# Kernel optimization log

Hardware: AMD Instinct MI355X
Metric: run time of the kernel (lower is better)

## Reference

```python
import jax, jax.numpy as jnp
import numpy as np
import math

B, N, F0, HID, OUT, K = 8, 2048, 128, 64, 16, 10


def setup_inputs() -> dict:
    key = jax.random.key(0)
    ks = jax.random.split(key, 6)
    X = jax.random.normal(ks[0], (B, N, F0), dtype=jnp.float32)
    # Row-stochastic dense 'rescaled Laplacian': spectrum inside unit disk,
    # so K-th order Bernstein polynomial stays numerically stable.
    A = jax.random.uniform(ks[1], (N, N), dtype=jnp.float32)
    L = A / jnp.sum(A, axis=1, keepdims=True)
    W1 = jax.random.normal(ks[2], (F0, HID), dtype=jnp.float32) / np.float32(np.sqrt(F0))
    b1 = jnp.zeros((HID,), dtype=jnp.float32)
    W2 = jax.random.normal(ks[3], (HID, OUT), dtype=jnp.float32) / np.float32(np.sqrt(HID))
    b2 = jnp.zeros((OUT,), dtype=jnp.float32)
    theta = 0.02 * jax.random.normal(ks[4], (K + 1,), dtype=jnp.float32)
    return {"X": X, "L": L, "W1": W1, "b1": b1, "W2": W2, "b2": b2,
            "theta": theta, "dp": 0}


def _bern_filter(Hf, L, theta, binom):
    # g(L) Hf = sum_i theta_i C(K,i) L^i (I-L)^{K-i} Hf
    # Computed by applying L / (I-L) directly to the (B,N,F) features
    # (mathematically identical to forming the NxN basis matrices).
    Lap = lambda Y: jnp.einsum('vw,bwf->bvf', L, Y)
    ys = [Hf]                       # ys[k] = (I-L)^k Hf
    for _ in range(K):
        ys.append(ys[-1] - Lap(ys[-1]))
    a = theta * binom               # (K+1,)
    # Horner in L: r = a_K Hf; r <- L r + a_i (I-L)^{K-i} Hf
    r = a[K] * Hf
    for i in range(K - 1, -1, -1):
        r = Lap(r) + a[i] * ys[K - i]
    return r


def reference(X, L, W1, b1, W2, b2, theta, dp):
    binom = jnp.asarray([math.comb(K, i) for i in range(K + 1)], dtype=X.dtype)
    # dropout with p=dp=0 is identity
    Hf = jax.nn.relu(X @ W1 + b1)          # (B, N, HID)
    Hf = _bern_filter(Hf, L, theta, binom) # (B, N, HID)
    Hg = jnp.mean(Hf, axis=1)              # (B, HID)
    logits = Hg @ W2 + b2                  # (B, OUT)
    return logits
```

## Files before the change

kernel.cpp:

```cpp
#include <hip/hip_runtime.h>

#define NN     2048
#define F0D    128
#define HIDD   64
#define OUTD   16
#define KDEG   10
#define NCHAIN 128
#define COLS   16

typedef unsigned long long u64;
typedef unsigned int u32;

#define CTAG(j) (0xC0DE0000u + (u32)(j))
#define HTAG    0xBEEF0001u

static __device__ __forceinline__ u64 ld_ag(const u64* p) {
    return __hip_atomic_load(p, __ATOMIC_RELAXED, __HIP_MEMORY_SCOPE_AGENT);
}
static __device__ __forceinline__ void st_ag(u64* p, u64 v) {
    __hip_atomic_store(p, v, __ATOMIC_RELAXED, __HIP_MEMORY_SCOPE_AGENT);
}
static __device__ __forceinline__ u64 pk(u32 tag, float x) {
    return ((u64)tag << 32) | (u64)__float_as_uint(x);
}


__global__ __launch_bounds__(256, 1) void k_fused(
    const float* __restrict__ X, const float* __restrict__ L,
    const float* __restrict__ W1, const float* __restrict__ b1,
    const float* __restrict__ W2, const float* __restrict__ b2,
    const float* __restrict__ theta, float* __restrict__ out,
    float* __restrict__ ws)
{
    u64* bpW0  = (u64*)ws;
    u64* bpW1  = bpW0 + NN;
    u64* weffW = bpW0 + 2 * NN;
    u64* HpW   = bpW0 + 3 * NN;

    __shared__ union {
        struct { float Lt[NN * COLS]; float xs[NN]; float redf[4][16]; float cbv[16]; } mv;
        struct { float W1t[64][132]; float redm[16][65]; float wv[64]; } hd;
    } sm;

    const int g = blockIdx.x;
    const int t = threadIdx.x;

    if (g < NCHAIN) {
        const int u0 = g * COLS;

        if (t <= KDEG) {
            const float C10[11] = {1,10,45,120,210,252,210,120,45,10,1};
            float acc = 0.f;
            for (int i = 0; i <= t; ++i) {
                int n = KDEG - i, r = t - i;
                long long cm = 1;
                for (int s = 1; s <= r; ++s) cm = cm * (n - r + s) / s;
                float term = theta[i] * C10[i] * (float)cm;
                if ((t - i) & 1) term = -term;
                acc += term;
            }
            sm.mv.cbv[t] = acc;
        }

        const float4* L4  = (const float4*)L;
        float4*       Lt4 = (float4*)sm.mv.Lt;
        #pragma unroll 16
        for (int i = 0; i < 32; ++i) {
            int idx = t + 256 * i;
            int v = idx >> 2, qc = idx & 3;
            Lt4[idx] = L4[(size_t)v * (NN / 4) + (u0 >> 2) + qc];
        }
        __syncthreads();

        float wacc = 0.f;
        for (int j = 1; j <= KDEG; ++j) {
            float pprev = 1.0f;
            if (j > 1) {
                const u64* src = ((j - 1) & 1) ? bpW1 : bpW0;
                const u32 tag = CTAG(j - 1);
                const int base = t * 8;
                u64 vb[8];
                u32 need = 0xFFu;
                while (need) {
                    #pragma unroll
                    for (int i = 0; i < 8; ++i) {
                        if (need & (1u << i)) {
                            u64 x = ld_ag(&src[base + i]);
                            if ((u32)(x >> 32) == tag) { vb[i] = x; need &= ~(1u << i); }
                        }
                    }
                    if (need) __builtin_amdgcn_s_sleep(1);
                }
                #pragma unroll
                for (int i = 0; i < 8; ++i)
                    sm.mv.xs[base + i] = __uint_as_float((u32)vb[i]);
                __syncthreads();
                if (t < COLS) pprev = sm.mv.xs[u0 + t];
            }

            const int qc = t & 3, r = t >> 2;
            float4 acc = make_float4(0.f, 0.f, 0.f, 0.f);
            #pragma unroll 8
            for (int k = 0; k < 32; ++k) {
                int v = r + 64 * k;
                float xv = (j == 1) ? 1.0f : sm.mv.xs[v];
                float4 lv = Lt4[v * 4 + qc];
                acc.x += lv.x * xv; acc.y += lv.y * xv;
                acc.z += lv.z * xv; acc.w += lv.w * xv;
            }
            #pragma unroll
            for (int m = 4; m <= 32; m <<= 1) {
                acc.x += __shfl_xor(acc.x, m); acc.y += __shfl_xor(acc.y, m);
                acc.z += __shfl_xor(acc.z, m); acc.w += __shfl_xor(acc.w, m);
            }
            int lane = t & 63, wid = t >> 6;
            if (lane < 4) *(float4*)&sm.mv.redf[wid][lane * 4] = acc;
            __syncthreads();

            if (t < COLS) {
                float s = sm.mv.redf[0][t] + sm.mv.redf[1][t]
                        + sm.mv.redf[2][t] + sm.mv.redf[3][t];
                wacc += sm.mv.cbv[j - 1] * pprev;
                if (j < KDEG) {
                    u64* dst = (j & 1) ? bpW1 : bpW0;
                    st_ag(&dst[u0 + t], pk(CTAG(j), s));
                } else {
                    st_ag(&weffW[u0 + t],
                          pk(CTAG(KDEG), wacc + sm.mv.cbv[KDEG] * s));
                }
            }
        }

        if (g == 0) {
            const float inv = 1.0f / (float)NN;
            float s2[2];
            const int idx0 = t * 2;
            #pragma unroll
            for (int e = 0; e < 2; ++e) {
                int idx = idx0 + e;
                int b = idx >> 6, h = idx & 63;
                const u64* base = &HpW[(size_t)(b * 32) * 64 + h];
                u32 rem = 0xFFFFFFFFu;
                float ssum = 0.f;
                while (rem) {
                    for (int vc = 0; vc < 32; ++vc) {
                        if (rem & (1u << vc)) {
                            u64 x = ld_ag(base + (size_t)vc * 64);
                            if ((u32)(x >> 32) == HTAG) {
                                ssum += __uint_as_float((u32)x);
                                rem &= ~(1u << vc);
                            }
                        }
                    }
                    if (rem) __builtin_amdgcn_s_sleep(4);
                }
                s2[e] = ssum * inv;
            }
            sm.mv.xs[idx0] = s2[0];
            sm.mv.xs[idx0 + 1] = s2[1];
            __syncthreads();
            if (t < 128) {
                int o = t & 15, bb = t >> 4;
                float a3 = b2[o];
                #pragma unroll
                for (int h = 0; h < HIDD; ++h)
                    a3 += sm.mv.xs[bb * 64 + h] * W2[h * 16 + o];
                out[bb * 16 + o] = a3;
            }
        }
        return;
    }

    const int u = g - NCHAIN;
    const int vchunk = u & 31, bA = u >> 5, bB = bA + 4;

    for (int i = t; i < F0D * HIDD; i += 256) {
        int f = i >> 6, h = i & 63;
        sm.hd.W1t[h][f] = W1[i];
    }
    __syncthreads();

    const int hg = t & 15, vg = t >> 4;
    const int vbase = vchunk * 64 + vg * 4;
    const float* XA = X + ((size_t)bA * NN + vbase) * F0D;
    const float* XB = X + ((size_t)bB * NN + vbase) * F0D;
    float accA[4][4] = {}, accB[4][4] = {};
    for (int f = 0; f < F0D; f += 4) {
        float4 xa[4], xb[4];
        #pragma unroll
        for (int i = 0; i < 4; ++i) {
            xa[i] = *(const float4*)(XA + (size_t)i * F0D + f);
            xb[i] = *(const float4*)(XB + (size_t)i * F0D + f);
        }
        #pragma unroll
        for (int jj = 0; jj < 4; ++jj) {
            float4 wr = *(const float4*)(&sm.hd.W1t[hg + 16 * jj][f]);
            #pragma unroll
            for (int i = 0; i < 4; ++i) {
                accA[i][jj] += xa[i].x * wr.x + xa[i].y * wr.y
                             + xa[i].z * wr.z + xa[i].w * wr.w;
                accB[i][jj] += xb[i].x * wr.x + xb[i].y * wr.y
                             + xb[i].z * wr.z + xb[i].w * wr.w;
            }
        }
    }

    if (t < 64) {
        const u64* wp = &weffW[vchunk * 64 + t];
        u64 x = ld_ag(wp);
        while ((u32)(x >> 32) != CTAG(KDEG)) {
            __builtin_amdgcn_s_sleep(16);
            x = ld_ag(wp);
        }
        sm.hd.wv[t] = __uint_as_float((u32)x);
    }
    __syncthreads();

    float hsA[4] = {0.f,0.f,0.f,0.f}, hsB[4] = {0.f,0.f,0.f,0.f};
    #pragma unroll
    for (int i = 0; i < 4; ++i) {
        float we = sm.hd.wv[vg * 4 + i];
        #pragma unroll
        for (int jj = 0; jj < 4; ++jj) {
            float rA = accA[i][jj] + b1[hg + 16 * jj];
            float rB = accB[i][jj] + b1[hg + 16 * jj];
            rA = rA > 0.f ? rA : 0.f;
            rB = rB > 0.f ? rB : 0.f;
            hsA[jj] += rA * we;
            hsB[jj] += rB * we;
        }
    }
    #pragma unroll
    for (int jj = 0; jj < 4; ++jj) sm.hd.redm[vg][hg + 16 * jj] = hsA[jj];
    __syncthreads();
    if (t < 64) {
        float s = 0.f;
        #pragma unroll
        for (int i = 0; i < 16; ++i) s += sm.hd.redm[i][t];
        st_ag(&HpW[(size_t)(bA * 32 + vchunk) * 64 + t], pk(HTAG, s));
    }
    __syncthreads();
    #pragma unroll
    for (int jj = 0; jj < 4; ++jj) sm.hd.redm[vg][hg + 16 * jj] = hsB[jj];
    __syncthreads();
    if (t < 64) {
        float s = 0.f;
        #pragma unroll
        for (int i = 0; i < 16; ++i) s += sm.hd.redm[i][t];
        st_ag(&HpW[(size_t)(bB * 32 + vchunk) * 64 + t], pk(HTAG, s));
    }
}

extern "C" void kernel_launch(void* const* d_in, const int* in_sizes, int n_in,
                              void* d_out, int out_size, void* d_ws, size_t ws_size,
                              hipStream_t stream) {
    const float* X     = (const float*)d_in[0];
    const float* L     = (const float*)d_in[1];
    const float* W1    = (const float*)d_in[2];
    const float* b1    = (const float*)d_in[3];
    const float* W2    = (const float*)d_in[4];
    const float* b2    = (const float*)d_in[5];
    const float* theta = (const float*)d_in[6];
    float* outp = (float*)d_out;
    float* wsp  = (float*)d_ws;

    hipLaunchKernelGGL(k_fused, dim3(256), dim3(256), 0, stream,
                       X, L, W1, b1, W2, b2, theta, outp, wsp);
}
```

Baseline: 140.4 us.

## Replace tagged 64-bit value polling with per-block flags and plain data buffers

Cross-block communication changes from packing a tag into every 64-bit value and polling every element to writing plain floats and then one release flag per block. Consumers poll 128 flags and then bulk-load the data vector with float4 loads. The first chain step (L times a ones vector) is folded into the L tile load, and each iteration gets its own buffer, so double-buffer aliasing goes away. This relies on relaxed stores plus s_waitcnt for ordering, which could be a memory-model risk, since there is no explicit release fence.

Measured after the change: 123.4 us. 12.1% less time.

```diff
diff --git a/kernel.cpp b/kernel.cpp
--- a/kernel.cpp
+++ b/kernel.cpp
@@ -8,22 +8,20 @@
 #define NCHAIN 128
 #define COLS   16
 
-typedef unsigned long long u64;
 typedef unsigned int u32;
 
 #define CTAG(j) (0xC0DE0000u + (u32)(j))
 #define HTAG    0xBEEF0001u
 
-static __device__ __forceinline__ u64 ld_ag(const u64* p) {
+static __device__ __forceinline__ u32 ld_flag(const u32* p) {
     return __hip_atomic_load(p, __ATOMIC_RELAXED, __HIP_MEMORY_SCOPE_AGENT);
 }
-static __device__ __forceinline__ void st_ag(u64* p, u64 v) {
+static __device__ __forceinline__ void st_flag(u32* p, u32 v) {
     __hip_atomic_store(p, v, __ATOMIC_RELAXED, __HIP_MEMORY_SCOPE_AGENT);
 }
-static __device__ __forceinline__ u64 pk(u32 tag, float x) {
-    return ((u64)tag << 32) | (u64)__float_as_uint(x);
-}
-
+static __device__ __forceinline__ void st_data(float* p, float v) {
+    __hip_atomic_store(p, v, __ATOMIC_RELAXED, __HIP_MEMORY_SCOPE_AGENT);
+}
 
 __global__ __launch_bounds__(256, 1) void k_fused(
     const float* __restrict__ X, const float* __restrict__ L,
@@ -32,10 +30,10 @@
     const float* __restrict__ theta, float* __restrict__ out,
     float* __restrict__ ws)
 {
-    u64* bpW0  = (u64*)ws;
-    u64* bpW1  = bpW0 + NN;
-    u64* weffW = bpW0 + 2 * NN;
-    u64* HpW   = bpW0 + 3 * NN;
+    float* PB  = ws;
+    float* HP  = ws + 20480;
+    u32*   FLC = (u32*)(ws + 28672);
+    u32*   FLH = (u32*)(ws + 49152);
 
     __shared__ union {
         struct { float Lt[NN * COLS]; float xs[NN]; float redf[4][16]; float cbv[16]; } mv;
@@ -64,100 +62,122 @@
 
         const float4* L4  = (const float4*)L;
         float4*       Lt4 = (float4*)sm.mv.Lt;
-        #pragma unroll 16
+        const int qc = t & 3, r0 = t >> 2;
+        float4 acc = make_float4(0.f, 0.f, 0.f, 0.f);
+        #pragma unroll 8
         for (int i = 0; i < 32; ++i) {
-            int idx = t + 256 * i;
-            int v = idx >> 2, qc = idx & 3;
-            Lt4[idx] = L4[(size_t)v * (NN / 4) + (u0 >> 2) + qc];
+            int v = r0 + 64 * i;
+            float4 lv = L4[(size_t)v * (NN / 4) + (u0 >> 2) + qc];
+            Lt4[v * 4 + qc] = lv;
+            acc.x += lv.x; acc.y += lv.y; acc.z += lv.z; acc.w += lv.w;
+        }
+        #pragma unroll
+        for (int m = 4; m <= 32; m <<= 1) {
+            acc.x += __shfl_xor(acc.x, m); acc.y += __shfl_xor(acc.y, m);
+            acc.z += __shfl_xor(acc.z, m); acc.w += __shfl_xor(acc.w, m);
+        }
+        {
+            int lane = t & 63, wid = t >> 6;
+            if (lane < 4) *(float4*)&sm.mv.redf[wid][lane * 4] = acc;
         }
         __syncthreads();
 
         float wacc = 0.f;
-        for (int j = 1; j <= KDEG; ++j) {
-            float pprev = 1.0f;
-            if (j > 1) {
-                const u64* src = ((j - 1) & 1) ? bpW1 : bpW0;
+        if (t < COLS) {
+            float s = sm.mv.redf[0][t] + sm.mv.redf[1][t]
+                    + sm.mv.redf[2][t] + sm.mv.redf[3][t];
+            wacc = sm.mv.cbv[0];
+            st_data(&PB[u0 + t], s);
+        }
+        if (t < 64) {
+            asm volatile("s_waitcnt vmcnt(0)" ::: "memory");
+            if (t == 0) st_flag(((u32*)(ws + 28672)) + g * 16, CTAG(1));
+        }
+
+        for (int j = 2; j <= KDEG; ++j) {
+            if (t < 32) {
+                const u32* fb = (u32*)(ws + 28672 + (size_t)(j - 2) * 2048);
                 const u32 tag = CTAG(j - 1);
-                const int base = t * 8;
-                u64 vb[8];
-                u32 need = 0xFFu;
+                u32 need = 0xFu;
                 while (need) {
                     #pragma unroll
-                    for (int i = 0; i < 8; ++i) {
-                        if (need & (1u << i)) {
-                            u64 x = ld_ag(&src[base + i]);
-                            if ((u32)(x >> 32) == tag) { vb[i] = x; need &= ~(1u << i); }
-                        }
-                    }
+                    for (int i = 0; i < 4; ++i)
+                        if (need & (1u << i))
+                            if (ld_flag(fb + (t + 32 * i) * 16) == tag)
+                                need &= ~(1u << i);
                     if (need) __builtin_amdgcn_s_sleep(1);
                 }
-                #pragma unroll
-                for (int i = 0; i < 8; ++i)
-                    sm.mv.xs[base + i] = __uint_as_float((u32)vb[i]);
-                __syncthreads();
-                if (t < COLS) pprev = sm.mv.xs[u0 + t];
-            }
-
-            const int qc = t & 3, r = t >> 2;
-            float4 acc = make_float4(0.f, 0.f, 0.f, 0.f);
+            }
+            __syncthreads();
+
+            const float4* src4 = (const float4*)(PB + (size_t)(j - 2) * 2048);
+            float4* xs4 = (float4*)sm.mv.xs;
+            xs4[t]       = src4[t];
+            xs4[t + 256] = src4[t + 256];
+            __syncthreads();
+
+            float pprev = (t < COLS) ? sm.mv.xs[u0 + t] : 0.f;
+
+            float4 a2 = make_float4(0.f, 0.f, 0.f, 0.f);
             #pragma unroll 8
             for (int k = 0; k < 32; ++k) {
-                int v = r + 64 * k;
-                float xv = (j == 1) ? 1.0f : sm.mv.xs[v];
+                int v = r0 + 64 * k;
+                float xv = sm.mv.xs[v];
                 float4 lv = Lt4[v * 4 + qc];
-                acc.x += lv.x * xv; acc.y += lv.y * xv;
-                acc.z += lv.z * xv; acc.w += lv.w * xv;
+                a2.x += lv.x * xv; a2.y += lv.y * xv;
+                a2.z += lv.z * xv; a2.w += lv.w * xv;
             }
             #pragma unroll
             for (int m = 4; m <= 32; m <<= 1) {
-                acc.x += __shfl_xor(acc.x, m); acc.y += __shfl_xor(acc.y, m);
-                acc.z += __shfl_xor(acc.z, m); acc.w += __shfl_xor(acc.w, m);
-            }
-            int lane = t & 63, wid = t >> 6;
-            if (lane < 4) *(float4*)&sm.mv.redf[wid][lane * 4] = acc;
+                a2.x += __shfl_xor(a2.x, m); a2.y += __shfl_xor(a2.y, m);
+                a2.z += __shfl_xor(a2.z, m); a2.w += __shfl_xor(a2.w, m);
+            }
+            {
+                int lane = t & 63, wid = t >> 6;
+                if (lane < 4) *(float4*)&sm.mv.redf[wid][lane * 4] = a2;
+            }
             __syncthreads();
 
             if (t < COLS) {
                 float s = sm.mv.redf[0][t] + sm.mv.redf[1][t]
                         + sm.mv.redf[2][t] + sm.mv.redf[3][t];
                 wacc += sm.mv.cbv[j - 1] * pprev;
-                if (j < KDEG) {
-                    u64* dst = (j & 1) ? bpW1 : bpW0;
-                    st_ag(&dst[u0 + t], pk(CTAG(j), s));
-                } else {
-                    st_ag(&weffW[u0 + t],
-                          pk(CTAG(KDEG), wacc + sm.mv.cbv[KDEG] * s));
+                float val = (j < KDEG) ? s : (wacc + sm.mv.cbv[KDEG] * s);
+                st_data(&PB[(size_t)(j - 1) * 2048 + u0 + t], val);
+            }
+            if (t < 64) {
+                asm volatile("s_waitcnt vmcnt(0)" ::: "memory");
+                if (t == 0)
+                    st_flag(((u32*)(ws + 28672 + (size_t)(j - 1) * 2048)) + g * 16,
+                            CTAG(j));
+            }
+        }
+
+        if (g == 0) {
+            if (t < 32) {
+                u32 need = 0xFu;
+                while (need) {
+                    #pragma unroll
+                    for (int i = 0; i < 4; ++i)
+                        if (need & (1u << i))
+                            if (ld_flag(FLH + (t + 32 * i) * 16) == HTAG)
+                                need &= ~(1u << i);
+                    if (need) __builtin_amdgcn_s_sleep(2);
                 }
             }
-        }
-
-        if (g == 0) {
-            const float inv = 1.0f / (float)NN;
+            __syncthreads();
             float s2[2];
-            const int idx0 = t * 2;
             #pragma unroll
             for (int e = 0; e < 2; ++e) {
-                int idx = idx0 + e;
-                int b = idx >> 6, h = idx & 63;
-                const u64* base = &HpW[(size_t)(b * 32) * 64 + h];
-                u32 rem = 0xFFFFFFFFu;
-                float ssum = 0.f;
-                while (rem) {
-                    for (int vc = 0; vc < 32; ++vc) {
-                        if (rem & (1u << vc)) {
-                            u64 x = ld_ag(base + (size_t)vc * 64);
-                            if ((u32)(x >> 32) == HTAG) {
-                                ssum += __uint_as_float((u32)x);
-                                rem &= ~(1u << vc);
-                            }
-                        }
-                    }
-                    if (rem) __builtin_amdgcn_s_sleep(4);
-                }
-                s2[e] = ssum * inv;
-            }
-            sm.mv.xs[idx0] = s2[0];
-            sm.mv.xs[idx0 + 1] = s2[1];
+                int idx = t * 2 + e, b = idx >> 6, h = idx & 63;
+                const float* hp = HP + (size_t)(b * 32) * 64 + h;
+                float ss = 0.f;
+                #pragma unroll
+                for (int vc = 0; vc < 32; ++vc) ss += hp[vc * 64];
+                s2[e] = ss;
+            }
+            sm.mv.xs[t * 2]     = s2[0];
+            sm.mv.xs[t * 2 + 1] = s2[1];
             __syncthreads();
             if (t < 128) {
                 int o = t & 15, bb = t >> 4;
@@ -205,17 +225,18 @@
         }
     }
 
-    if (t < 64) {
-        const u64* wp = &weffW[vchunk * 64 + t];
-        u64 x = ld_ag(wp);
-        while ((u32)(x >> 32) != CTAG(KDEG)) {
-            __builtin_amdgcn_s_sleep(16);
-            x = ld_ag(wp);
-        }
-        sm.hd.wv[t] = __uint_as_float((u32)x);
-    }
-    __syncthreads();
-
+    if (t < 4) {
+        const u32* fp = ((u32*)(ws + 28672 + (size_t)(KDEG - 1) * 2048))
+                      + (vchunk * 4 + t) * 16;
+        while (ld_flag(fp) != CTAG(KDEG)) __builtin_amdgcn_s_sleep(2);
+    }
+    __syncthreads();
+    if (t < 16)
+        ((float4*)sm.hd.wv)[t] =
+            ((const float4*)(PB + (size_t)(KDEG - 1) * 2048 + vchunk * 64))[t];
+    __syncthreads();
+
+    const float inv = 1.0f / (float)NN;
     float hsA[4] = {0.f,0.f,0.f,0.f}, hsB[4] = {0.f,0.f,0.f,0.f};
     #pragma unroll
     for (int i = 0; i < 4; ++i) {
@@ -237,7 +258,7 @@
         float s = 0.f;
         #pragma unroll
         for (int i = 0; i < 16; ++i) s += sm.hd.redm[i][t];
-        st_ag(&HpW[(size_t)(bA * 32 + vchunk) * 64 + t], pk(HTAG, s));
+        st_data(&HP[(size_t)(bA * 32 + vchunk) * 64 + t], s * inv);
     }
     __syncthreads();
     #pragma unroll
@@ -247,7 +268,11 @@
         float s = 0.f;
         #pragma unroll
         for (int i = 0; i < 16; ++i) s += sm.hd.redm[i][t];
-        st_ag(&HpW[(size_t)(bB * 32 + vchunk) * 64 + t], pk(HTAG, s));
+        st_data(&HP[(size_t)(bB * 32 + vchunk) * 64 + t], s * inv);
+    }
+    if (t < 64) {
+        asm volatile("s_waitcnt vmcnt(0)" ::: "memory");
+        if (t == 0) st_flag(FLH + u * 16, HTAG);
     }
 }
 
```
